# Performance work log

Hardware: AMD Instinct MI355X
Metric: run time of the kernel (lower is better)

Reference implementation:

```python
import jax, jax.numpy as jnp
import numpy as np

T, H, O, R, A = 8192, 4096, 4096, 16, 8

def setup_inputs() -> dict:
    key = jax.random.key(0)
    k1, k2, k3, k4, k5 = jax.random.split(key, 5)
    return {
        "result": jax.random.normal(k1, (T, O), dtype=jnp.float32),
        "x": jax.random.normal(k2, (T, H), dtype=jnp.float32),
        "lora_a": jax.random.normal(k3, (A, H, R), dtype=jnp.float32) * 0.02,
        "lora_b": jax.random.normal(k4, (A, R, O), dtype=jnp.float32) * 0.02,
        "adapter_indices": jax.random.randint(k5, (T,), 0, A, dtype=jnp.int32),
    }

def reference(result, x, lora_a, lora_b, adapter_indices):
    # Multi-adapter LoRA: result += sum_a mask_a * ((x @ A_a) @ B_a)
    n_adapters = lora_a.shape[0]
    # shrink: [T, A, R] -- low-rank projection for every adapter
    v = jnp.einsum('th,ahr->tar', x, lora_a)
    # per-token adapter mask (equivalent to adapter_mask in forward_lora)
    onehot = (adapter_indices[:, None] == jnp.arange(n_adapters)[None, :]).astype(x.dtype)
    v = v * onehot[:, :, None]
    # expand and accumulate into shared result tensor
    out = result + jnp.einsum('tar,aro->to', v, lora_b)
    return out
```

## Files before the change

kernel.cpp:

```cpp
#include <hip/hip_runtime.h>

#define T_TOK 8192
#define H_DIM 4096
#define O_DIM 4096
#define R_RANK 16
#define N_AD 8

#define TB_S 32
#define HC 256
#define TB_E 32
#define OB 1024

__global__ void sort_kernel(const int* __restrict__ idx,
                            int* __restrict__ list, int* __restrict__ base) {
    __shared__ int cnt[N_AD], cur[N_AD];
    const int tid = threadIdx.x;
    if (tid < N_AD) cnt[tid] = 0;
    __syncthreads();
    for (int t = tid; t < T_TOK; t += blockDim.x) atomicAdd(&cnt[idx[t]], 1);
    __syncthreads();
    if (tid == 0) {
        int s = 0;
        for (int a = 0; a < N_AD; ++a) { base[a] = s; cur[a] = s; s += cnt[a]; }
        base[N_AD] = s;
    }
    __syncthreads();
    for (int t = tid; t < T_TOK; t += blockDim.x) {
        int slot = atomicAdd(&cur[idx[t]], 1);
        list[slot] = t;
    }
}

__global__ __launch_bounds__(256, 2) void shrink_kernel(
    const float* __restrict__ x, const float* __restrict__ lora_a,
    const int* __restrict__ list, const int* __restrict__ base,
    float* __restrict__ V) {
    const int a = blockIdx.z;
    const int s0 = base[a], s1 = base[a + 1];
    const int start = s0 + blockIdx.x * TB_S;
    if (start >= s1) return;
    const int nt = min(TB_S, s1 - start);

    __shared__ float x_t[TB_S][HC + 1];
    __shared__ float a_t[HC][20];
    __shared__ float red2[4][8][4][16];
    __shared__ int toks[TB_S];

    const int tid = threadIdx.x;
    const int hs = tid >> 3;
    const int tg = tid & 7;

    if (tid < TB_S) toks[tid] = (tid < nt) ? list[start + tid] : -1;
    __syncthreads();

    float vacc[4][16];
    #pragma unroll
    for (int i = 0; i < 4; ++i)
        #pragma unroll
        for (int r = 0; r < 16; ++r) vacc[i][r] = 0.f;

    const float* Abase = lora_a + (size_t)a * H_DIM * R_RANK;

    for (int h0 = 0; h0 < H_DIM; h0 += HC) {
        #pragma unroll
        for (int k = 0; k < 8; ++k) {
            int flat = k * 256 + tid;
            int row = flat >> 6, col4 = flat & 63;
            int t = toks[row];
            float4 vx = make_float4(0.f, 0.f, 0.f, 0.f);
            if (t >= 0) vx = *(const float4*)&x[(size_t)t * H_DIM + h0 + (col4 << 2)];
            float* dst = &x_t[row][col4 << 2];
            dst[0] = vx.x; dst[1] = vx.y; dst[2] = vx.z; dst[3] = vx.w;
        }
        #pragma unroll
        for (int k = 0; k < 4; ++k) {
            int flat = k * 256 + tid;
            int h = flat >> 2, q = flat & 3;
            *(float4*)&a_t[h][q << 2] =
                *(const float4*)&Abase[(size_t)(h0 + h) * R_RANK + (q << 2)];
        }
        __syncthreads();

        #pragma unroll
        for (int hh = 0; hh < 8; ++hh) {
            const int h = (hh << 5) + hs;
            const float4 a0 = *(const float4*)&a_t[h][0];
            const float4 a1 = *(const float4*)&a_t[h][4];
            const float4 a2 = *(const float4*)&a_t[h][8];
            const float4 a3 = *(const float4*)&a_t[h][12];
            #pragma unroll
            for (int i = 0; i < 4; ++i) {
                const float xv = x_t[(tg << 2) + i][h];
                vacc[i][0]  += xv * a0.x; vacc[i][1]  += xv * a0.y;
                vacc[i][2]  += xv * a0.z; vacc[i][3]  += xv * a0.w;
                vacc[i][4]  += xv * a1.x; vacc[i][5]  += xv * a1.y;
                vacc[i][6]  += xv * a1.z; vacc[i][7]  += xv * a1.w;
                vacc[i][8]  += xv * a2.x; vacc[i][9]  += xv * a2.y;
                vacc[i][10] += xv * a2.z; vacc[i][11] += xv * a2.w;
                vacc[i][12] += xv * a3.x; vacc[i][13] += xv * a3.y;
                vacc[i][14] += xv * a3.z; vacc[i][15] += xv * a3.w;
            }
        }
        __syncthreads();
    }

    #pragma unroll
    for (int i = 0; i < 4; ++i)
        #pragma unroll
        for (int r = 0; r < 16; ++r) {
            float f = vacc[i][r];
            f += __shfl_xor(f, 8);
            f += __shfl_xor(f, 16);
            f += __shfl_xor(f, 32);
            vacc[i][r] = f;
        }
    const int lane = tid & 63, w = tid >> 6;
    if ((lane >> 3) == 0) {
        #pragma unroll
        for (int i = 0; i < 4; ++i)
            #pragma unroll
            for (int q = 0; q < 4; ++q)
                *(float4*)&red2[w][tg][i][q << 2] =
                    make_float4(vacc[i][(q << 2)], vacc[i][(q << 2) + 1],
                                vacc[i][(q << 2) + 2], vacc[i][(q << 2) + 3]);
    }
    __syncthreads();
    if (tid < 128) {
        const int tl = tid >> 2, q = tid & 3;
        const int tg2 = tl >> 2, i2 = tl & 3;
        float4 s = make_float4(0.f, 0.f, 0.f, 0.f);
        #pragma unroll
        for (int w2 = 0; w2 < 4; ++w2) {
            const float4 p = *(const float4*)&red2[w2][tg2][i2][q << 2];
            s.x += p.x; s.y += p.y; s.z += p.z; s.w += p.w;
        }
        const int t = toks[tl];
        if (t >= 0) *(float4*)&V[(size_t)t * R_RANK + (q << 2)] = s;
    }
}

__global__ __launch_bounds__(256, 2) void expand_kernel(
    const float* __restrict__ result, const float* __restrict__ lora_b,
    const float* __restrict__ V, const int* __restrict__ list,
    const int* __restrict__ base, float* __restrict__ out) {
    const int a = blockIdx.z;
    const int s0 = base[a], s1 = base[a + 1];
    const int start = s0 + blockIdx.x * TB_E;
    if (start >= s1) return;
    const int nt = min(TB_E, s1 - start);
    const int tid = threadIdx.x;

    __shared__ float v_lds[TB_E][16];
    __shared__ int toks[TB_E];
    if (tid < TB_E) toks[tid] = (tid < nt) ? list[start + tid] : -1;
    __syncthreads();
    if (tid < 128) {
        const int tl = tid >> 2, q = tid & 3;
        const int t = toks[tl];
        float4 val = make_float4(0.f, 0.f, 0.f, 0.f);
        if (t >= 0) val = *(const float4*)&V[(size_t)t * R_RANK + (q << 2)];
        *(float4*)&v_lds[tl][q << 2] = val;
    }

    const size_t o0 = (size_t)blockIdx.y * OB + ((size_t)tid << 2);
    const float* Bb = lora_b + (size_t)a * R_RANK * O_DIM + o0;
    float4 b[16];
    #pragma unroll
    for (int r = 0; r < 16; ++r) b[r] = *(const float4*)&Bb[(size_t)r * O_DIM];
    __syncthreads();

    for (int tl = 0; tl < nt; ++tl) {
        const int t = toks[tl];
        float4 acc = *(const float4*)&result[(size_t)t * O_DIM + o0];
        float vs[16];
        #pragma unroll
        for (int q = 0; q < 4; ++q)
            *(float4*)&vs[q << 2] = *(const float4*)&v_lds[tl][q << 2];
        #pragma unroll
        for (int r = 0; r < 16; ++r) {
            acc.x += vs[r] * b[r].x; acc.y += vs[r] * b[r].y;
            acc.z += vs[r] * b[r].z; acc.w += vs[r] * b[r].w;
        }
        *(float4*)&out[(size_t)t * O_DIM + o0] = acc;
    }
}

extern "C" void kernel_launch(void* const* d_in, const int* in_sizes, int n_in,
                              void* d_out, int out_size, void* d_ws, size_t ws_size,
                              hipStream_t stream) {
    const float* result = (const float*)d_in[0];
    const float* x      = (const float*)d_in[1];
    const float* lora_a = (const float*)d_in[2];
    const float* lora_b = (const float*)d_in[3];
    const int*   aidx   = (const int*)d_in[4];
    float* out = (float*)d_out;

    float* V   = (float*)d_ws;
    int* list  = (int*)((char*)d_ws + (size_t)T_TOK * R_RANK * 4);
    int* base  = (int*)((char*)list + (size_t)T_TOK * 4);

    sort_kernel<<<1, 256, 0, stream>>>(aidx, list, base);
    shrink_kernel<<<dim3((T_TOK + TB_S - 1) / TB_S, 1, N_AD), 256, 0, stream>>>(
        x, lora_a, list, base, V);
    expand_kernel<<<dim3((T_TOK + TB_E - 1) / TB_E, O_DIM / OB, N_AD), 256, 0, stream>>>(
        result, lora_b, V, list, base, out);
}
```

Before: 431.3 us.

## Parallelize token sort, split shrink over H, and unroll expand by two tokens

Replaces the single-block sort with a multi-block ballot-based histogram, a scan and a scatter, so the serial sort no longer stalls the pipeline. The shrink kernel is split four ways along H (smaller HC chunks, more blocks, higher occupancy bound), writing partial V slices that expand sums when it loads V. Expand processes two tokens per iteration for more memory-level parallelism. This adds extra launches, a memset and four times the V workspace traffic.

```diff
diff --git a/kernel.cpp b/kernel.cpp
--- a/kernel.cpp
+++ b/kernel.cpp
@@ -7,34 +7,53 @@
 #define N_AD 8
 
 #define TB_S 32
-#define HC 256
+#define HC 128
+#define HSPLIT 4
+#define HRANGE (H_DIM / HSPLIT)
 #define TB_E 32
 #define OB 1024
 
-__global__ void sort_kernel(const int* __restrict__ idx,
-                            int* __restrict__ list, int* __restrict__ base) {
-    __shared__ int cnt[N_AD], cur[N_AD];
-    const int tid = threadIdx.x;
-    if (tid < N_AD) cnt[tid] = 0;
-    __syncthreads();
-    for (int t = tid; t < T_TOK; t += blockDim.x) atomicAdd(&cnt[idx[t]], 1);
-    __syncthreads();
-    if (tid == 0) {
-        int s = 0;
-        for (int a = 0; a < N_AD; ++a) { base[a] = s; cur[a] = s; s += cnt[a]; }
-        base[N_AD] = s;
-    }
-    __syncthreads();
-    for (int t = tid; t < T_TOK; t += blockDim.x) {
-        int slot = atomicAdd(&cur[idx[t]], 1);
-        list[slot] = t;
-    }
-}
-
-__global__ __launch_bounds__(256, 2) void shrink_kernel(
+__global__ void hist_kernel(const int* __restrict__ idx, int* __restrict__ cnt) {
+    const int t = blockIdx.x * 256 + threadIdx.x;
+    const int a = idx[t];
+    const int lane = threadIdx.x & 63;
+    #pragma unroll
+    for (int k = 0; k < N_AD; ++k) {
+        unsigned long long m = __ballot(a == k);
+        if (lane == 0 && m) atomicAdd(&cnt[k], (int)__popcll(m));
+    }
+}
+
+__global__ void scan_kernel(const int* __restrict__ cnt, int* __restrict__ base,
+                            int* __restrict__ cur) {
+    int s = 0;
+    #pragma unroll
+    for (int a = 0; a < N_AD; ++a) { base[a] = s; cur[a] = s; s += cnt[a]; }
+    base[N_AD] = s;
+}
+
+__global__ void scatter_kernel(const int* __restrict__ idx, int* __restrict__ cur,
+                               int* __restrict__ list) {
+    const int t = blockIdx.x * 256 + threadIdx.x;
+    const int a = idx[t];
+    const int lane = threadIdx.x & 63;
+    const unsigned long long lt_mask = (1ull << lane) - 1ull;
+    #pragma unroll
+    for (int k = 0; k < N_AD; ++k) {
+        unsigned long long m = __ballot(a == k);
+        if (m) {
+            int s = 0;
+            if (lane == 0) s = atomicAdd(&cur[k], (int)__popcll(m));
+            s = __shfl(s, 0);
+            if (a == k) list[s + (int)__popcll(m & lt_mask)] = t;
+        }
+    }
+}
+
+__global__ __launch_bounds__(256, 4) void shrink_kernel(
     const float* __restrict__ x, const float* __restrict__ lora_a,
     const int* __restrict__ list, const int* __restrict__ base,
-    float* __restrict__ V) {
+    float* __restrict__ V4) {
     const int a = blockIdx.z;
     const int s0 = base[a], s1 = base[a + 1];
     const int start = s0 + blockIdx.x * TB_S;
@@ -49,6 +68,7 @@
     const int tid = threadIdx.x;
     const int hs = tid >> 3;
     const int tg = tid & 7;
+    const int hb = blockIdx.y * HRANGE;
 
     if (tid < TB_S) toks[tid] = (tid < nt) ? list[start + tid] : -1;
     __syncthreads();
@@ -61,11 +81,12 @@
 
     const float* Abase = lora_a + (size_t)a * H_DIM * R_RANK;
 
-    for (int h0 = 0; h0 < H_DIM; h0 += HC) {
-        #pragma unroll
-        for (int k = 0; k < 8; ++k) {
+    for (int c = 0; c < HRANGE / HC; ++c) {
+        const int h0 = hb + c * HC;
+        #pragma unroll
+        for (int k = 0; k < 4; ++k) {
             int flat = k * 256 + tid;
-            int row = flat >> 6, col4 = flat & 63;
+            int row = flat >> 5, col4 = flat & 31;
             int t = toks[row];
             float4 vx = make_float4(0.f, 0.f, 0.f, 0.f);
             if (t >= 0) vx = *(const float4*)&x[(size_t)t * H_DIM + h0 + (col4 << 2)];
@@ -73,7 +94,7 @@
             dst[0] = vx.x; dst[1] = vx.y; dst[2] = vx.z; dst[3] = vx.w;
         }
         #pragma unroll
-        for (int k = 0; k < 4; ++k) {
+        for (int k = 0; k < 2; ++k) {
             int flat = k * 256 + tid;
             int h = flat >> 2, q = flat & 3;
             *(float4*)&a_t[h][q << 2] =
@@ -82,7 +103,7 @@
         __syncthreads();
 
         #pragma unroll
-        for (int hh = 0; hh < 8; ++hh) {
+        for (int hh = 0; hh < HC / 32; ++hh) {
             const int h = (hh << 5) + hs;
             const float4 a0 = *(const float4*)&a_t[h][0];
             const float4 a1 = *(const float4*)&a_t[h][4];
@@ -135,13 +156,14 @@
             s.x += p.x; s.y += p.y; s.z += p.z; s.w += p.w;
         }
         const int t = toks[tl];
-        if (t >= 0) *(float4*)&V[(size_t)t * R_RANK + (q << 2)] = s;
-    }
-}
-
-__global__ __launch_bounds__(256, 2) void expand_kernel(
+        if (t >= 0)
+            *(float4*)&V4[((size_t)blockIdx.y * T_TOK + t) * R_RANK + (q << 2)] = s;
+    }
+}
+
+__global__ __launch_bounds__(256, 4) void expand_kernel(
     const float* __restrict__ result, const float* __restrict__ lora_b,
-    const float* __restrict__ V, const int* __restrict__ list,
+    const float* __restrict__ V4, const int* __restrict__ list,
     const int* __restrict__ base, float* __restrict__ out) {
     const int a = blockIdx.z;
     const int s0 = base[a], s1 = base[a + 1];
@@ -157,9 +179,16 @@
     if (tid < 128) {
         const int tl = tid >> 2, q = tid & 3;
         const int t = toks[tl];
-        float4 val = make_float4(0.f, 0.f, 0.f, 0.f);
-        if (t >= 0) val = *(const float4*)&V[(size_t)t * R_RANK + (q << 2)];
-        *(float4*)&v_lds[tl][q << 2] = val;
+        float4 s = make_float4(0.f, 0.f, 0.f, 0.f);
+        if (t >= 0) {
+            #pragma unroll
+            for (int sp = 0; sp < HSPLIT; ++sp) {
+                const float4 p = *(const float4*)
+                    &V4[((size_t)sp * T_TOK + t) * R_RANK + (q << 2)];
+                s.x += p.x; s.y += p.y; s.z += p.z; s.w += p.w;
+            }
+        }
+        *(float4*)&v_lds[tl][q << 2] = s;
     }
 
     const size_t o0 = (size_t)blockIdx.y * OB + ((size_t)tid << 2);
@@ -169,19 +198,32 @@
     for (int r = 0; r < 16; ++r) b[r] = *(const float4*)&Bb[(size_t)r * O_DIM];
     __syncthreads();
 
-    for (int tl = 0; tl < nt; ++tl) {
-        const int t = toks[tl];
-        float4 acc = *(const float4*)&result[(size_t)t * O_DIM + o0];
-        float vs[16];
-        #pragma unroll
-        for (int q = 0; q < 4; ++q)
-            *(float4*)&vs[q << 2] = *(const float4*)&v_lds[tl][q << 2];
+    int tl = 0;
+    for (; tl + 2 <= nt; tl += 2) {
+        const int t0 = toks[tl], t1 = toks[tl + 1];
+        float4 acc0 = *(const float4*)&result[(size_t)t0 * O_DIM + o0];
+        float4 acc1 = *(const float4*)&result[(size_t)t1 * O_DIM + o0];
         #pragma unroll
         for (int r = 0; r < 16; ++r) {
-            acc.x += vs[r] * b[r].x; acc.y += vs[r] * b[r].y;
-            acc.z += vs[r] * b[r].z; acc.w += vs[r] * b[r].w;
-        }
-        *(float4*)&out[(size_t)t * O_DIM + o0] = acc;
+            const float v0 = v_lds[tl][r], v1 = v_lds[tl + 1][r];
+            acc0.x += v0 * b[r].x; acc0.y += v0 * b[r].y;
+            acc0.z += v0 * b[r].z; acc0.w += v0 * b[r].w;
+            acc1.x += v1 * b[r].x; acc1.y += v1 * b[r].y;
+            acc1.z += v1 * b[r].z; acc1.w += v1 * b[r].w;
+        }
+        *(float4*)&out[(size_t)t0 * O_DIM + o0] = acc0;
+        *(float4*)&out[(size_t)t1 * O_DIM + o0] = acc1;
+    }
+    if (tl < nt) {
+        const int t0 = toks[tl];
+        float4 acc0 = *(const float4*)&result[(size_t)t0 * O_DIM + o0];
+        #pragma unroll
+        for (int r = 0; r < 16; ++r) {
+            const float v0 = v_lds[tl][r];
+            acc0.x += v0 * b[r].x; acc0.y += v0 * b[r].y;
+            acc0.z += v0 * b[r].z; acc0.w += v0 * b[r].w;
+        }
+        *(float4*)&out[(size_t)t0 * O_DIM + o0] = acc0;
     }
 }
 
@@ -195,13 +237,20 @@
     const int*   aidx   = (const int*)d_in[4];
     float* out = (float*)d_out;
 
-    float* V   = (float*)d_ws;
-    int* list  = (int*)((char*)d_ws + (size_t)T_TOK * R_RANK * 4);
-    int* base  = (int*)((char*)list + (size_t)T_TOK * 4);
-
-    sort_kernel<<<1, 256, 0, stream>>>(aidx, list, base);
-    shrink_kernel<<<dim3((T_TOK + TB_S - 1) / TB_S, 1, N_AD), 256, 0, stream>>>(
-        x, lora_a, list, base, V);
-    expand_kernel<<<dim3((T_TOK + TB_E - 1) / TB_E, O_DIM / OB, N_AD), 256, 0, stream>>>(
-        result, lora_b, V, list, base, out);
-}
+    char* ws = (char*)d_ws;
+    float* V4  = (float*)ws;
+    size_t off = (size_t)HSPLIT * T_TOK * R_RANK * 4;
+    int* list  = (int*)(ws + off);   off += (size_t)T_TOK * 4;
+    int* base  = (int*)(ws + off);   off += 16 * 4;
+    int* cnt   = (int*)(ws + off);   off += 16 * 4;
+    int* cur   = (int*)(ws + off);
+
+    hipMemsetAsync(cnt, 0, N_AD * sizeof(int), stream);
+    hist_kernel<<<T_TOK / 256, 256, 0, stream>>>(aidx, cnt);
+    scan_kernel<<<1, 1, 0, stream>>>(cnt, base, cur);
+    scatter_kernel<<<T_TOK / 256, 256, 0, stream>>>(aidx, cur, list);
+    shrink_kernel<<<dim3(T_TOK / TB_S, HSPLIT, N_AD), 256, 0, stream>>>(
+        x, lora_a, list, base, V4);
+    expand_kernel<<<dim3(T_TOK / TB_E, O_DIM / OB, N_AD), 256, 0, stream>>>(
+        result, lora_b, V4, list, base, out);
+}
```

After: 475.4 us. +10.2%, slower.
